# Performance work log

Measured on AMD Instinct MI355X. Metric: run time of the kernel, lower is better.

Reference implementation:

```python
import jax, jax.numpy as jnp
import numpy as np

D_MODEL = 1024
NUM_HEADS = 16
HEAD_DIM = D_MODEL // NUM_HEADS
B, L = 2, 2048


def setup_inputs() -> dict:
    key = jax.random.key(0)
    ks = jax.random.split(key, 9)
    s = 0.02
    return {
        "query": jax.random.normal(ks[0], (B, L, D_MODEL), dtype=jnp.float32),
        "key": jax.random.normal(ks[1], (B, L, D_MODEL), dtype=jnp.float32),
        "value": jax.random.normal(ks[2], (B, L, D_MODEL), dtype=jnp.float32),
        "mask": jax.random.randint(ks[3], (B, L), 0, 2, dtype=jnp.int32),
        "Wq": jax.random.normal(ks[4], (D_MODEL, D_MODEL), dtype=jnp.float32) * s,
        "Wk": jax.random.normal(ks[5], (D_MODEL, D_MODEL), dtype=jnp.float32) * s,
        "Wv": jax.random.normal(ks[6], (D_MODEL, D_MODEL), dtype=jnp.float32) * s,
        "Wo": jax.random.normal(ks[7], (D_MODEL, D_MODEL), dtype=jnp.float32) * s,
        "bo": jnp.zeros((D_MODEL,), dtype=jnp.float32),
    }


def _split_heads(x):
    # (B, L, d_model) -> (B, H, L, head_dim)
    b, l, _ = x.shape
    return x.reshape(b, l, NUM_HEADS, HEAD_DIM).transpose(0, 2, 1, 3)


def reference(query, key, value, mask, Wq, Wk, Wv, Wo, bo):
    # nn.Linear(bias=False): x @ W.T
    q = _split_heads(query @ Wq.T)   # (B, H, L, hd)
    k = _split_heads(key @ Wk.T)
    v = _split_heads(value @ Wv.T)

    scores = jnp.einsum("bhqd,bhkd->bhqk", q, k) / jnp.sqrt(jnp.float32(HEAD_DIM))
    # padding mask over keys: (B, L) -> (B, 1, 1, L); 0 = pad -> -inf
    keep = (mask[:, None, None, :] != 0)
    scores = jnp.where(keep, scores, -jnp.inf)

    attn = jax.nn.softmax(scores, axis=-1)
    # original zeroes NaN rows (fully-masked query rows)
    attn = jnp.where(jnp.isnan(attn), jnp.zeros_like(attn), attn)
    # dropout is identity in eval/reference mode

    ctx = jnp.einsum("bhqk,bhkd->bhqd", attn, v)           # (B, H, L, hd)
    ctx = ctx.transpose(0, 2, 1, 3).reshape(B, L, D_MODEL)  # combine heads
    return ctx @ Wo.T + bo
```

## Files before the change

### kernel.cpp

```cpp
#include <hip/hip_runtime.h>

typedef unsigned short u16;
typedef __bf16 bf16x8 __attribute__((ext_vector_type(8)));
typedef __bf16 bf16x4 __attribute__((ext_vector_type(4)));
typedef float floatx4 __attribute__((ext_vector_type(4)));
typedef u16 u16x4 __attribute__((ext_vector_type(4)));

#define MEG ((size_t)(1u << 20))

__device__ __forceinline__ u16 f2bf(float f) {
  unsigned int u = __float_as_uint(f);
  u += 0x7fffu + ((u >> 16) & 1u);
  return (u16)(u >> 16);
}
__device__ __forceinline__ unsigned pk2(float a, float b) {
  return (unsigned)f2bf(a) | ((unsigned)f2bf(b) << 16);
}

__device__ __forceinline__ void load_lds16(const u16* g, u16* l) {
  __builtin_amdgcn_global_load_lds((const __attribute__((address_space(1))) unsigned int*)g,
                                   (__attribute__((address_space(3))) unsigned int*)l,
                                   16, 0, 0);
}

__global__ __launch_bounds__(256) void cvt7(
    const float* __restrict__ s0, const float* __restrict__ s1,
    const float* __restrict__ s2, const float* __restrict__ s3,
    const float* __restrict__ s4, const float* __restrict__ s5,
    const float* __restrict__ s6, u16* __restrict__ dst)
{
  size_t e = ((size_t)blockIdx.x * 256 + threadIdx.x) * 4;
  unsigned m = (unsigned)(e >> 20);
  const float* s; size_t off;
  if (m < 4)       { s = s0; off = e; }
  else if (m < 8)  { s = s1; off = e - 4 * MEG; }
  else if (m < 12) { s = s2; off = e - 8 * MEG; }
  else if (m < 13) { s = s3; off = e - 12 * MEG; }
  else if (m < 14) { s = s4; off = e - 13 * MEG; }
  else if (m < 15) { s = s5; off = e - 14 * MEG; }
  else             { s = s6; off = e - 15 * MEG; }
  float4 f = *reinterpret_cast<const float4*>(s + off);
  u16x4 o;
  o.x = f2bf(f.x); o.y = f2bf(f.y); o.z = f2bf(f.z); o.w = f2bf(f.w);
  *reinterpret_cast<u16x4*>(dst + e) = o;
}

template<bool OUT_BF16, bool ADD_BIAS>
__global__ __launch_bounds__(256) void gemm_bt(
    const u16* __restrict__ Abase, const u16* __restrict__ Bbase,
    const float* __restrict__ bias, void* __restrict__ Cbase,
    int M, int N, int K, long zA, long zB, long zC)
{
  __shared__ __align__(16) u16 As[128 * 32];
  __shared__ __align__(16) u16 Bs[128 * 32];
  const int tid = threadIdx.x;
  const int w = tid >> 6, ln = tid & 63;
  const int lm = ln & 15, lq = ln >> 4;
  const int wm = w >> 1, wn = w & 1;
  const long m0 = (long)blockIdx.y * 128, n0 = (long)blockIdx.x * 128;
  const u16* A = Abase + (size_t)blockIdx.z * (size_t)zA;
  const u16* B = Bbase + (size_t)blockIdx.z * (size_t)zB;

  const floatx4 z4 = {0.f, 0.f, 0.f, 0.f};
  floatx4 acc[4][4];
#pragma unroll
  for (int i = 0; i < 4; ++i)
#pragma unroll
    for (int j = 0; j < 4; ++j) acc[i][j] = z4;

  for (int k0 = 0; k0 < K; k0 += 32) {
#pragma unroll
    for (int rr = 0; rr < 2; ++rr) {
      int c = rr * 256 + tid;
      long row = c >> 2; int cg = c & 3;
      load_lds16(A + (m0 + row) * K + k0 + cg * 8, &As[(rr * 256 + w * 64) * 8]);
      load_lds16(B + (n0 + row) * K + k0 + cg * 8, &Bs[(rr * 256 + w * 64) * 8]);
    }
    __syncthreads();
    bf16x8 af[4], bfr[4];
#pragma unroll
    for (int i = 0; i < 4; ++i)
      af[i] = *reinterpret_cast<const bf16x8*>(&As[(wm * 64 + i * 16 + lm) * 32 + lq * 8]);
#pragma unroll
    for (int j = 0; j < 4; ++j)
      bfr[j] = *reinterpret_cast<const bf16x8*>(&Bs[(wn * 64 + j * 16 + lm) * 32 + lq * 8]);
#pragma unroll
    for (int i = 0; i < 4; ++i)
#pragma unroll
      for (int j = 0; j < 4; ++j)
        acc[i][j] = __builtin_amdgcn_mfma_f32_16x16x32_bf16(af[i], bfr[j], acc[i][j], 0, 0, 0);
    __syncthreads();
  }

#pragma unroll
  for (int i = 0; i < 4; ++i) {
    long row = m0 + wm * 64 + i * 16 + lq * 4;
#pragma unroll
    for (int j = 0; j < 4; ++j) {
      long col = n0 + wn * 64 + j * 16 + lm;
#pragma unroll
      for (int r = 0; r < 4; ++r) {
        float v = acc[i][j][r];
        if (ADD_BIAS) v += bias[col];
        size_t idx = (size_t)(row + r) * (size_t)N + (size_t)col;
        if (OUT_BF16) (((u16*)Cbase) + (size_t)blockIdx.z * (size_t)zC)[idx] = f2bf(v);
        else ((float*)Cbase)[idx] = v;
      }
    }
  }
}

__global__ __launch_bounds__(256) void transpose_v(const u16* __restrict__ Vp, u16* __restrict__ Vt)
{
  __shared__ u16 T[64 * 80];
  const int tid = threadIdx.x;
  const int bh = blockIdx.y, b = bh >> 4, h = bh & 15;
  const int l0 = blockIdx.x * 64;
#pragma unroll
  for (int t = 0; t < 2; ++t) {
    int ci = t * 256 + tid;
    int l = ci >> 3, c = ci & 7;
    *reinterpret_cast<uint4*>(&T[l * 80 + c * 8]) =
      *reinterpret_cast<const uint4*>(&Vp[((size_t)(b * 2048 + l0 + l)) * 1024 + h * 64 + c * 8]);
  }
  __syncthreads();
#pragma unroll
  for (int t = 0; t < 2; ++t) {
    int ci = t * 256 + tid;
    int d = ci >> 3, lg = ci & 7;
    u16 tmp[8];
#pragma unroll
    for (int s = 0; s < 8; ++s) tmp[s] = T[(lg * 8 + s) * 80 + d];
    *reinterpret_cast<uint4*>(&Vt[(size_t)bh * 131072 + (size_t)d * 2048 + l0 + lg * 8]) =
      *reinterpret_cast<uint4*>(tmp);
  }
}

__global__ __launch_bounds__(256) void attn_kernel(
    const u16* __restrict__ Qp, const u16* __restrict__ Kp,
    const u16* __restrict__ Vt, const int* __restrict__ mask,
    u16* __restrict__ ctx)
{
  __shared__ __align__(16) u16 Ks[64 * 64];
  __shared__ __align__(16) u16 Vts[64 * 64];
  __shared__ __align__(16) u16 Ps[4 * 16 * 64];
  __shared__ __align__(16) float mb[64];

  const int tid = threadIdx.x;
  const int w = tid >> 6, ln = tid & 63;
  const int lm = ln & 15, lq = ln >> 4;
  const int bh = blockIdx.y, b = bh >> 4, h = bh & 15;
  const int q0 = blockIdx.x * 64;

  const u16* Qh = Qp + (size_t)b * 2048 * 1024 + h * 64;
  const u16* Kh = Kp + (size_t)b * 2048 * 1024 + h * 64;
  const u16* Vth = Vt + (size_t)bh * 64 * 2048;

  const int qrow = q0 + w * 16 + lm;
  bf16x8 qf[2];
#pragma unroll
  for (int h2 = 0; h2 < 2; ++h2)
    qf[h2] = *reinterpret_cast<const bf16x8*>(Qh + (size_t)qrow * 1024 + h2 * 32 + lq * 8);

  const floatx4 z4 = {0.f, 0.f, 0.f, 0.f};
  floatx4 O[4];
#pragma unroll
  for (int j = 0; j < 4; ++j) O[j] = z4;
  float psum = 0.f;

  u16* Pw = &Ps[w * 1024];
  const float SCL = 0.18033688011112042f;

  for (int k0 = 0; k0 < 2048; k0 += 64) {
#pragma unroll
    for (int t = 0; t < 2; ++t) {
      int ci = t * 256 + tid;
      int row = ci >> 3, s = ci & 7;
      int kc = s ^ (row & 7);
      load_lds16(Kh + (size_t)(k0 + row) * 1024 + kc * 8, &Ks[(t * 256 + w * 64) * 8]);
      load_lds16(Vth + (size_t)row * 2048 + k0 + kc * 8, &Vts[(t * 256 + w * 64) * 8]);
    }
    if (tid < 64) mb[tid] = (mask[b * 2048 + k0 + tid] != 0) ? 0.f : -1e30f;
    __syncthreads();

    bf16x8 kf[4][2], vf[4][2];
#pragma unroll
    for (int n = 0; n < 4; ++n) {
      int key = n * 16 + lm;
#pragma unroll
      for (int h2 = 0; h2 < 2; ++h2) {
        int slot = (h2 * 4 + lq) ^ (key & 7);
        kf[n][h2] = *reinterpret_cast<const bf16x8*>(&Ks[key * 64 + slot * 8]);
      }
    }
#pragma unroll
    for (int j = 0; j < 4; ++j) {
      int d = j * 16 + lm;
#pragma unroll
      for (int h2 = 0; h2 < 2; ++h2) {
        int slot = (h2 * 4 + lq) ^ (d & 7);
        vf[j][h2] = *reinterpret_cast<const bf16x8*>(&Vts[d * 64 + slot * 8]);
      }
    }

    floatx4 S[4];
#pragma unroll
    for (int n = 0; n < 4; ++n) {
      S[n] = __builtin_amdgcn_mfma_f32_16x16x32_bf16(kf[n][0], qf[0], z4, 0, 0, 0);
      S[n] = __builtin_amdgcn_mfma_f32_16x16x32_bf16(kf[n][1], qf[1], S[n], 0, 0, 0);
    }

#pragma unroll
    for (int n = 0; n < 4; ++n) {
      float4 mbf = *reinterpret_cast<const float4*>(&mb[n * 16 + lq * 4]);
      float p0 = exp2f(S[n][0] * SCL + mbf.x);
      float p1 = exp2f(S[n][1] * SCL + mbf.y);
      float p2 = exp2f(S[n][2] * SCL + mbf.z);
      float p3 = exp2f(S[n][3] * SCL + mbf.w);
      psum += (p0 + p1) + (p2 + p3);
      uint2 pkd = make_uint2(pk2(p0, p1), pk2(p2, p3));
      int sp = (4 * n + lq) ^ lm;
      *reinterpret_cast<uint2*>(&Pw[lm * 64 + sp * 4]) = pkd;
    }

#pragma unroll
    for (int h2 = 0; h2 < 2; ++h2) {
      int s0 = 8 * h2 + 2 * lq;
      bf16x4 pa = *reinterpret_cast<const bf16x4*>(&Pw[lm * 64 + (s0 ^ lm) * 4]);
      bf16x4 pb = *reinterpret_cast<const bf16x4*>(&Pw[lm * 64 + ((s0 + 1) ^ lm) * 4]);
      bf16x8 pf = __builtin_shufflevector(pa, pb, 0, 1, 2, 3, 4, 5, 6, 7);
#pragma unroll
      for (int j = 0; j < 4; ++j)
        O[j] = __builtin_amdgcn_mfma_f32_16x16x32_bf16(pf, vf[j][h2], O[j], 0, 0, 0);
    }
    __syncthreads();
  }

  float s = psum;
  s += __shfl_xor(s, 16, 64);
  s += __shfl_xor(s, 32, 64);
#pragma unroll
  for (int r = 0; r < 4; ++r) {
    int srcl = (ln & 48) | (lq * 4 + r);
    float inv = 1.0f / __shfl(s, srcl, 64);
    int row = q0 + w * 16 + lq * 4 + r;
    size_t base = ((size_t)b * 2048 + row) * 1024 + h * 64 + lm;
#pragma unroll
    for (int j = 0; j < 4; ++j)
      ctx[base + j * 16] = f2bf(O[j][r] * inv);
  }
}

extern "C" void kernel_launch(void* const* d_in, const int* in_sizes, int n_in,
                              void* d_out, int out_size, void* d_ws, size_t ws_size,
                              hipStream_t stream) {
  const float* q  = (const float*)d_in[0];
  const float* k  = (const float*)d_in[1];
  const float* v  = (const float*)d_in[2];
  const int*   mk = (const int*)  d_in[3];
  const float* wq = (const float*)d_in[4];
  const float* wk = (const float*)d_in[5];
  const float* wv = (const float*)d_in[6];
  const float* wo = (const float*)d_in[7];
  const float* bo = (const float*)d_in[8];

  u16* ws16 = (u16*)d_ws;
  u16* Xq  = ws16;
  u16* Wq  = ws16 + 12 * MEG;
  u16* Wo  = ws16 + 15 * MEG;
  u16* Qp  = ws16 + 16 * MEG;
  u16* Kp  = ws16 + 20 * MEG;
  u16* Vp  = ws16 + 24 * MEG;
  u16* Vt  = ws16;
  u16* ctx = ws16 + 4 * MEG;

  cvt7<<<dim3(16384), dim3(256), 0, stream>>>(q, k, v, wq, wk, wv, wo, ws16);

  gemm_bt<true, false><<<dim3(8, 32, 3), dim3(256), 0, stream>>>(
      Xq, Wq, nullptr, (void*)Qp, 4096, 1024, 1024,
      (long)(4 * MEG), (long)MEG, (long)(4 * MEG));

  transpose_v<<<dim3(32, 32), dim3(256), 0, stream>>>(Vp, Vt);

  attn_kernel<<<dim3(32, 32), dim3(256), 0, stream>>>(Qp, Kp, Vt, mk, ctx);

  gemm_bt<false, true><<<dim3(8, 32, 1), dim3(256), 0, stream>>>(
      ctx, Wo, bo, d_out, 4096, 1024, 1024, 0, 0, 0);
}
```

Baseline: 261.0 us.

## Widen GEMM K-tile with swizzled LDS and streamline attention inner loop

The GEMM now stages a 64-wide K tile per iteration using XOR-swizzled LDS layout and precomputed pointers, halving barrier count per K. The attention kernel preloads the whole mask row into LDS once, hoists address computation out of the loop, uses the hardware exp2 intrinsic with fma, replaces round-to-nearest-even bf16 conversion with cheaper round-half-up via perm, and adds a launch-bounds occupancy hint. The risks are higher LDS usage (8KB mask buffer plus doubled GEMM tiles) that may lower occupancy, and slightly different rounding of probabilities.

```diff
diff --git a/kernel.cpp b/kernel.cpp
--- a/kernel.cpp
+++ b/kernel.cpp
@@ -12,9 +12,6 @@
   unsigned int u = __float_as_uint(f);
   u += 0x7fffu + ((u >> 16) & 1u);
   return (u16)(u >> 16);
-}
-__device__ __forceinline__ unsigned pk2(float a, float b) {
-  return (unsigned)f2bf(a) | ((unsigned)f2bf(b) << 16);
 }
 
 __device__ __forceinline__ void load_lds16(const u16* g, u16* l) {
@@ -51,8 +48,8 @@
     const float* __restrict__ bias, void* __restrict__ Cbase,
     int M, int N, int K, long zA, long zB, long zC)
 {
-  __shared__ __align__(16) u16 As[128 * 32];
-  __shared__ __align__(16) u16 Bs[128 * 32];
+  __shared__ __align__(16) u16 As[128 * 64];
+  __shared__ __align__(16) u16 Bs[128 * 64];
   const int tid = threadIdx.x;
   const int w = tid >> 6, ln = tid & 63;
   const int lm = ln & 15, lq = ln >> 4;
@@ -61,6 +58,19 @@
   const u16* A = Abase + (size_t)blockIdx.z * (size_t)zA;
   const u16* B = Bbase + (size_t)blockIdx.z * (size_t)zB;
 
+  const int r0 = tid >> 3;
+  const int kc = (tid & 7) ^ (r0 & 7);
+  const u16* gA = A + (m0 + r0) * (long)K + kc * 8;
+  const u16* gB = B + (n0 + r0) * (long)K + kc * 8;
+  const long rstep = 32L * K;
+
+  const int sl0 = (lq ^ (lm & 7)) * 8;
+  const int sl1 = ((4 + lq) ^ (lm & 7)) * 8;
+  const u16* ab0 = &As[(wm * 64 + lm) * 64 + sl0];
+  const u16* ab1 = &As[(wm * 64 + lm) * 64 + sl1];
+  const u16* bb0 = &Bs[(wn * 64 + lm) * 64 + sl0];
+  const u16* bb1 = &Bs[(wn * 64 + lm) * 64 + sl1];
+
   const floatx4 z4 = {0.f, 0.f, 0.f, 0.f};
   floatx4 acc[4][4];
 #pragma unroll
@@ -68,27 +78,32 @@
 #pragma unroll
     for (int j = 0; j < 4; ++j) acc[i][j] = z4;
 
-  for (int k0 = 0; k0 < K; k0 += 32) {
-#pragma unroll
-    for (int rr = 0; rr < 2; ++rr) {
-      int c = rr * 256 + tid;
-      long row = c >> 2; int cg = c & 3;
-      load_lds16(A + (m0 + row) * K + k0 + cg * 8, &As[(rr * 256 + w * 64) * 8]);
-      load_lds16(B + (n0 + row) * K + k0 + cg * 8, &Bs[(rr * 256 + w * 64) * 8]);
-    }
+  for (int k0 = 0; k0 < K; k0 += 64) {
+#pragma unroll
+    for (int t = 0; t < 4; ++t) {
+      load_lds16(gA + t * rstep, &As[(t * 256 + w * 64) * 8]);
+      load_lds16(gB + t * rstep, &Bs[(t * 256 + w * 64) * 8]);
+    }
+    gA += 64; gB += 64;
     __syncthreads();
-    bf16x8 af[4], bfr[4];
+    bf16x8 af[4][2], bfr[4][2];
+#pragma unroll
+    for (int i = 0; i < 4; ++i) {
+      af[i][0] = *reinterpret_cast<const bf16x8*>(ab0 + i * 1024);
+      af[i][1] = *reinterpret_cast<const bf16x8*>(ab1 + i * 1024);
+    }
+#pragma unroll
+    for (int j = 0; j < 4; ++j) {
+      bfr[j][0] = *reinterpret_cast<const bf16x8*>(bb0 + j * 1024);
+      bfr[j][1] = *reinterpret_cast<const bf16x8*>(bb1 + j * 1024);
+    }
 #pragma unroll
     for (int i = 0; i < 4; ++i)
-      af[i] = *reinterpret_cast<const bf16x8*>(&As[(wm * 64 + i * 16 + lm) * 32 + lq * 8]);
-#pragma unroll
-    for (int j = 0; j < 4; ++j)
-      bfr[j] = *reinterpret_cast<const bf16x8*>(&Bs[(wn * 64 + j * 16 + lm) * 32 + lq * 8]);
-#pragma unroll
-    for (int i = 0; i < 4; ++i)
-#pragma unroll
-      for (int j = 0; j < 4; ++j)
-        acc[i][j] = __builtin_amdgcn_mfma_f32_16x16x32_bf16(af[i], bfr[j], acc[i][j], 0, 0, 0);
+#pragma unroll
+      for (int j = 0; j < 4; ++j) {
+        acc[i][j] = __builtin_amdgcn_mfma_f32_16x16x32_bf16(af[i][0], bfr[j][0], acc[i][j], 0, 0, 0);
+        acc[i][j] = __builtin_amdgcn_mfma_f32_16x16x32_bf16(af[i][1], bfr[j][1], acc[i][j], 0, 0, 0);
+      }
     __syncthreads();
   }
 
@@ -136,7 +151,7 @@
   }
 }
 
-__global__ __launch_bounds__(256) void attn_kernel(
+__global__ __launch_bounds__(256, 4) void attn_kernel(
     const u16* __restrict__ Qp, const u16* __restrict__ Kp,
     const u16* __restrict__ Vt, const int* __restrict__ mask,
     u16* __restrict__ ctx)
@@ -144,7 +159,7 @@
   __shared__ __align__(16) u16 Ks[64 * 64];
   __shared__ __align__(16) u16 Vts[64 * 64];
   __shared__ __align__(16) u16 Ps[4 * 16 * 64];
-  __shared__ __align__(16) float mb[64];
+  __shared__ __align__(16) float mball[2048];
 
   const int tid = threadIdx.x;
   const int w = tid >> 6, ln = tid & 63;
@@ -156,83 +171,99 @@
   const u16* Kh = Kp + (size_t)b * 2048 * 1024 + h * 64;
   const u16* Vth = Vt + (size_t)bh * 64 * 2048;
 
+  const int* mrow = mask + b * 2048;
+#pragma unroll
+  for (int t = 0; t < 8; ++t) {
+    int i = t * 256 + tid;
+    mball[i] = (mrow[i] != 0) ? 0.f : -1e30f;
+  }
+
   const int qrow = q0 + w * 16 + lm;
-  bf16x8 qf[2];
-#pragma unroll
-  for (int h2 = 0; h2 < 2; ++h2)
-    qf[h2] = *reinterpret_cast<const bf16x8*>(Qh + (size_t)qrow * 1024 + h2 * 32 + lq * 8);
+  bf16x8 qf0 = *reinterpret_cast<const bf16x8*>(Qh + (size_t)qrow * 1024 + lq * 8);
+  bf16x8 qf1 = *reinterpret_cast<const bf16x8*>(Qh + (size_t)qrow * 1024 + 32 + lq * 8);
+
+  const int sl0 = (lq ^ (lm & 7)) * 8;
+  const int sl1 = ((4 + lq) ^ (lm & 7)) * 8;
+  const u16* kb0 = &Ks[lm * 64 + sl0];
+  const u16* kb1 = &Ks[lm * 64 + sl1];
+  const u16* vb0 = &Vts[lm * 64 + sl0];
+  const u16* vb1 = &Vts[lm * 64 + sl1];
+  u16* Pw = &Ps[w * 1024];
+  u16* pwr[4];
+#pragma unroll
+  for (int n = 0; n < 4; ++n) pwr[n] = &Pw[lm * 64 + (((4 * n + lq) ^ lm) * 4)];
+  const u16* prd[4];
+#pragma unroll
+  for (int t = 0; t < 4; ++t)
+    prd[t] = &Pw[lm * 64 + (((8 * (t >> 1) + 2 * lq + (t & 1)) ^ lm) * 4)];
+  const float* mbi = mball + lq * 4;
+
+  const int r0 = tid >> 3;
+  const int kc = (tid & 7) ^ (r0 & 7);
+  const u16* gK0 = Kh + (size_t)r0 * 1024 + kc * 8;
+  const u16* gK1 = gK0 + 32 * 1024;
+  const u16* gV0 = Vth + (size_t)r0 * 2048 + kc * 8;
+  const u16* gV1 = gV0 + 32 * 2048;
 
   const floatx4 z4 = {0.f, 0.f, 0.f, 0.f};
   floatx4 O[4];
 #pragma unroll
   for (int j = 0; j < 4; ++j) O[j] = z4;
   float psum = 0.f;
-
-  u16* Pw = &Ps[w * 1024];
   const float SCL = 0.18033688011112042f;
 
-  for (int k0 = 0; k0 < 2048; k0 += 64) {
-#pragma unroll
-    for (int t = 0; t < 2; ++t) {
-      int ci = t * 256 + tid;
-      int row = ci >> 3, s = ci & 7;
-      int kc = s ^ (row & 7);
-      load_lds16(Kh + (size_t)(k0 + row) * 1024 + kc * 8, &Ks[(t * 256 + w * 64) * 8]);
-      load_lds16(Vth + (size_t)row * 2048 + k0 + kc * 8, &Vts[(t * 256 + w * 64) * 8]);
-    }
-    if (tid < 64) mb[tid] = (mask[b * 2048 + k0 + tid] != 0) ? 0.f : -1e30f;
+  for (int it = 0; it < 32; ++it) {
+    load_lds16(gK0, &Ks[(w * 64) * 8]);
+    load_lds16(gK1, &Ks[(256 + w * 64) * 8]);
+    load_lds16(gV0, &Vts[(w * 64) * 8]);
+    load_lds16(gV1, &Vts[(256 + w * 64) * 8]);
+    gK0 += 64 * 1024; gK1 += 64 * 1024; gV0 += 64; gV1 += 64;
     __syncthreads();
 
-    bf16x8 kf[4][2], vf[4][2];
+    bf16x8 kf[4][2];
 #pragma unroll
     for (int n = 0; n < 4; ++n) {
-      int key = n * 16 + lm;
-#pragma unroll
-      for (int h2 = 0; h2 < 2; ++h2) {
-        int slot = (h2 * 4 + lq) ^ (key & 7);
-        kf[n][h2] = *reinterpret_cast<const bf16x8*>(&Ks[key * 64 + slot * 8]);
+      kf[n][0] = *reinterpret_cast<const bf16x8*>(kb0 + n * 1024);
+      kf[n][1] = *reinterpret_cast<const bf16x8*>(kb1 + n * 1024);
+    }
+    floatx4 S[4];
+#pragma unroll
+    for (int n = 0; n < 4; ++n) {
+      S[n] = __builtin_amdgcn_mfma_f32_16x16x32_bf16(kf[n][0], qf0, z4, 0, 0, 0);
+      S[n] = __builtin_amdgcn_mfma_f32_16x16x32_bf16(kf[n][1], qf1, S[n], 0, 0, 0);
+    }
+
+#pragma unroll
+    for (int n = 0; n < 4; ++n) {
+      float4 m4 = *reinterpret_cast<const float4*>(mbi + n * 16);
+      float p0 = __builtin_amdgcn_exp2f(fmaf(S[n][0], SCL, m4.x));
+      float p1 = __builtin_amdgcn_exp2f(fmaf(S[n][1], SCL, m4.y));
+      float p2 = __builtin_amdgcn_exp2f(fmaf(S[n][2], SCL, m4.z));
+      float p3 = __builtin_amdgcn_exp2f(fmaf(S[n][3], SCL, m4.w));
+      psum += (p0 + p1) + (p2 + p3);
+      unsigned u0 = __float_as_uint(p0) + 0x8000u;
+      unsigned u1 = __float_as_uint(p1) + 0x8000u;
+      unsigned u2 = __float_as_uint(p2) + 0x8000u;
+      unsigned u3 = __float_as_uint(p3) + 0x8000u;
+      uint2 pk;
+      pk.x = __builtin_amdgcn_perm(u1, u0, 0x07060302u);
+      pk.y = __builtin_amdgcn_perm(u3, u2, 0x07060302u);
+      *reinterpret_cast<uint2*>(pwr[n]) = pk;
+    }
+
+#pragma unroll
+    for (int h2 = 0; h2 < 2; ++h2) {
+      bf16x4 pa = *reinterpret_cast<const bf16x4*>(prd[2 * h2]);
+      bf16x4 pb = *reinterpret_cast<const bf16x4*>(prd[2 * h2 + 1]);
+      bf16x8 pf = __builtin_shufflevector(pa, pb, 0, 1, 2, 3, 4, 5, 6, 7);
+      const u16* vb = (h2 == 0) ? vb0 : vb1;
+#pragma unroll
+      for (int j = 0; j < 4; ++j) {
+        bf16x8 vf = *reinterpret_cast<const bf16x8*>(vb + j * 1024);
+        O[j] = __builtin_amdgcn_mfma_f32_16x16x32_bf16(pf, vf, O[j], 0, 0, 0);
       }
     }
-#pragma unroll
-    for (int j = 0; j < 4; ++j) {
-      int d = j * 16 + lm;
-#pragma unroll
-      for (int h2 = 0; h2 < 2; ++h2) {
-        int slot = (h2 * 4 + lq) ^ (d & 7);
-        vf[j][h2] = *reinterpret_cast<const bf16x8*>(&Vts[d * 64 + slot * 8]);
-      }
-    }
-
-    floatx4 S[4];
-#pragma unroll
-    for (int n = 0; n < 4; ++n) {
-      S[n] = __builtin_amdgcn_mfma_f32_16x16x32_bf16(kf[n][0], qf[0], z4, 0, 0, 0);
-      S[n] = __builtin_amdgcn_mfma_f32_16x16x32_bf16(kf[n][1], qf[1], S[n], 0, 0, 0);
-    }
-
-#pragma unroll
-    for (int n = 0; n < 4; ++n) {
-      float4 mbf = *reinterpret_cast<const float4*>(&mb[n * 16 + lq * 4]);
-      float p0 = exp2f(S[n][0] * SCL + mbf.x);
-      float p1 = exp2f(S[n][1] * SCL + mbf.y);
-      float p2 = exp2f(S[n][2] * SCL + mbf.z);
-      float p3 = exp2f(S[n][3] * SCL + mbf.w);
-      psum += (p0 + p1) + (p2 + p3);
-      uint2 pkd = make_uint2(pk2(p0, p1), pk2(p2, p3));
-      int sp = (4 * n + lq) ^ lm;
-      *reinterpret_cast<uint2*>(&Pw[lm * 64 + sp * 4]) = pkd;
-    }
-
-#pragma unroll
-    for (int h2 = 0; h2 < 2; ++h2) {
-      int s0 = 8 * h2 + 2 * lq;
-      bf16x4 pa = *reinterpret_cast<const bf16x4*>(&Pw[lm * 64 + (s0 ^ lm) * 4]);
-      bf16x4 pb = *reinterpret_cast<const bf16x4*>(&Pw[lm * 64 + ((s0 + 1) ^ lm) * 4]);
-      bf16x8 pf = __builtin_shufflevector(pa, pb, 0, 1, 2, 3, 4, 5, 6, 7);
-#pragma unroll
-      for (int j = 0; j < 4; ++j)
-        O[j] = __builtin_amdgcn_mfma_f32_16x16x32_bf16(pf, vf[j][h2], O[j], 0, 0, 0);
-    }
+    mbi += 64;
     __syncthreads();
   }
 
```

Result: faster. 239.2 us (-8.4%).
